# Optimization experiments

Measured on AMD Instinct MI355X. Metric: run time of the kernel, lower is better.

## Reference

```python
import jax, jax.numpy as jnp
import numpy as np


def setup_inputs() -> dict:
    key = jax.random.key(0)
    k1, k2 = jax.random.split(key)
    flow = jax.random.normal(k1, (4, 2, 256, 256), dtype=jnp.float32)   # [B,2,H,W] per-pixel flow over dt
    spike = jax.random.uniform(k2, (4, 64, 256, 256), dtype=jnp.float32)  # [B,C,H,W] spike voxel grid
    return {"flow": flow, "spike": spike}


def _splat(vals, xn, yn, H, W):
    """Forward bilinear splat of vals [H,W] to continuous coords (xn,yn) [H,W]."""
    x0 = jnp.floor(xn)
    y0 = jnp.floor(yn)
    wx = xn - x0  # fractional weights (differentiable w.r.t. flow)
    wy = yn - y0
    x0i = x0.astype(jnp.int32)
    y0i = y0.astype(jnp.int32)
    out = jnp.zeros(H * W, dtype=vals.dtype)
    corners = (
        (0, 0, (1.0 - wx) * (1.0 - wy)),
        (1, 0, wx * (1.0 - wy)),
        (0, 1, (1.0 - wx) * wy),
        (1, 1, wx * wy),
    )
    for dx, dy, w in corners:
        xi = x0i + dx
        yi = y0i + dy
        valid = (xi >= 0) & (xi < W) & (yi >= 0) & (yi < H)
        idx = jnp.clip(yi, 0, H - 1) * W + jnp.clip(xi, 0, W - 1)
        out = out.at[idx.ravel()].add(jnp.where(valid, w * vals, 0.0).ravel())
    return out.reshape(H, W)


def spike_warp_mid(spike, flow, dt):
    """Warp each time bin c by flow * (c - mid)/dt toward the middle timestamp (bilinear splat)."""
    B, C, H, W = spike.shape
    mid = (C - 1) / 2.0
    yy, xx = jnp.meshgrid(jnp.arange(H, dtype=spike.dtype),
                          jnp.arange(W, dtype=spike.dtype), indexing='ij')
    s = (jnp.arange(C, dtype=spike.dtype) - mid) / jnp.asarray(dt, spike.dtype)  # [C]
    u = flow[:, 0][:, None]  # [B,1,H,W]
    v = flow[:, 1][:, None]
    xn = xx + u * s[None, :, None, None]  # [B,C,H,W]
    yn = yy + v * s[None, :, None, None]
    splat_bc = jax.vmap(jax.vmap(lambda va, xa, ya: _splat(va, xa, ya, H, W)))
    return splat_bc(spike, xn, yn)  # [B,C,H,W]


def reference(flow, spike):
    B, C, H, W = spike.shape
    spike_warped = spike_warp_mid(spike, flow, dt=64)
    # Faithful to original: sum over BATCH dim inside per-batch loop (same each iter),
    # so loss = (B * -var) / B = -var(spike_image) with unbiased variance.
    spike_image = jnp.sum(spike_warped, axis=0)  # [C,H,W]
    loss = -jnp.var(spike_image - jnp.mean(spike_image), ddof=1)
    return loss
```

## Files before the change

### kernel.cpp

```cpp
#include <hip/hip_runtime.h>

typedef float f2 __attribute__((ext_vector_type(2)));
typedef float f4v __attribute__((ext_vector_type(4)));

constexpr int B = 4, C = 64, H = 256, W = 256;
constexpr int HW = H * W;
constexpr long long N_TOT = (long long)C * HW;

constexpr int TW = 16, TH = 8;
constexpr int SWX = 24, SWY = 16;
constexpr int SA = SWX * SWY;
constexpr int INW = 18, INH = 10;
constexpr int INA = INW * INH;
constexpr int OVW = 17, OVH = 9;
constexpr int OVA = OVW * OVH;
constexpr int NTIL = 512;
constexpr int NBLK = NTIL * 8;

__global__ __launch_bounds__(128) void fused_kernel(
    const float* __restrict__ flow,
    const float* __restrict__ spike,
    double* __restrict__ partials) {
  __shared__ __align__(16) f4v pl01[INA];
  __shared__ __align__(16) f4v pl23[INA];
  __shared__ f2 uvp[INA];
  __shared__ __align__(16) float ovf[8 * OVA];
  __shared__ double red[4];

  const int bid = blockIdx.x;
  const int tile = bid >> 3;
  const int m = bid & 7;
  const int tx0 = (tile & 15) * TW;
  const int ty0 = (tile >> 4) * TH;
  const int tid = threadIdx.x;
  const int qx = tid & 15, qy = tid >> 4;
  const int wave = tid >> 6;

  {
    f4v z = {0.f, 0.f, 0.f, 0.f};
    f4v* ov4 = (f4v*)ovf;
    for (int i = tid; i < (8 * OVA) / 4; i += 128) ov4[i] = z;
  }

  f2 smv[4];
#pragma unroll
  for (int t = 0; t < 4; ++t) {
    float s = ((float)(m + 8 * t) + 0.5f) * (1.0f / 64.0f);
    smv[t] = f2{-s, s};
  }
  const int cno[4] = {31 - m, 23 - m, 15 - m, 7 - m};
  const int cpo[4] = {32 + m, 40 + m, 48 + m, 56 + m};

  const int sbg = (ty0 - 4) * W + (tx0 - 4);

  int c_rc[3], c_meta[3];
#pragma unroll
  for (int k = 0; k < 3; ++k) {
    int pos = tid + 128 * k;
    int row = pos / SWX;
    int col = pos - row * SWX;
    int relx = col - 4, rely = row - 4;
    int gy = ty0 + rely, gx = tx0 + relx;
    bool val = ((unsigned)gy < 256u) & ((unsigned)gx < 256u);
    bool i0 = ((unsigned)(relx + 1) < 18u) & ((unsigned)(rely + 1) < 10u);
    bool i1 = ((unsigned)(relx + 2) < 20u) & ((unsigned)(rely + 2) < 12u);
    bool i2 = ((unsigned)(relx + 3) < 22u) & ((unsigned)(rely + 3) < 14u);
    c_rc[k] = (row << 8) | col;
    c_meta[k] = (int)val | ((int)i1 << 1) | ((int)i2 << 2) | ((int)i0 << 3);
  }

  float p_u[3], p_v[3];
  float4 p_a[3], p_b[3];

  auto prefetch = [&](int bb) {
    const float* fu = flow + (size_t)bb * 2 * HW;
    const float* fv = fu + HW;
    const float* spb = spike + (size_t)bb * C * HW;
#pragma unroll
    for (int k = 0; k < 3; ++k) {
      const int meta = c_meta[k];
      float u = 0.f, v = 0.f;
      float4 a = {0.f, 0.f, 0.f, 0.f};
      float4 d = {0.f, 0.f, 0.f, 0.f};
      if (meta & 1) {
        const int gp = sbg + c_rc[k];
        u = fu[gp];
        v = fv[gp];
        d.z = spb[(size_t)cno[3] * HW + gp];
        d.w = spb[(size_t)cpo[3] * HW + gp];
        if (meta & 8) { a.x = spb[(size_t)cno[0] * HW + gp];
                        a.y = spb[(size_t)cpo[0] * HW + gp]; }
        if (meta & 2) { a.z = spb[(size_t)cno[1] * HW + gp];
                        a.w = spb[(size_t)cpo[1] * HW + gp]; }
        if (meta & 4) { d.x = spb[(size_t)cno[2] * HW + gp];
                        d.y = spb[(size_t)cpo[2] * HW + gp]; }
      }
      p_u[k] = u; p_v[k] = v; p_a[k] = a; p_b[k] = d;
    }
  };

  prefetch(0);
  __syncthreads();

  const int qb = (qy + 1) * INW + (qx + 1);
  f2 acc2[4];
#pragma unroll
  for (int t = 0; t < 4; ++t) acc2[t] = f2{0.f, 0.f};

  for (int bb = 0; bb < B; ++bb) {
#pragma unroll
    for (int k = 0; k < 3; ++k) {
      const int meta = c_meta[k];
      const float u = p_u[k], v = p_v[k];
      const float4 a = p_a[k], d = p_b[k];
      const float es = fmaxf(fabsf(u), fabsf(v));
      const bool ev0 = es * smv[0].y >= 1.0f;
      const bool ev1 = es * smv[1].y >= 1.0f;
      const bool ev2 = es * smv[2].y >= 1.0f;
      const bool ev3 = es * smv[3].y >= 1.0f;
      const int row = c_rc[k] >> 8, col = c_rc[k] & 255;
      if (meta & 8) {
        const int ips = (row - 3) * INW + (col - 3);
        uvp[ips] = f2{u, v};
        pl01[ips] = f4v{ev0 ? 0.f : a.x, ev0 ? 0.f : a.y,
                        ev1 ? 0.f : a.z, ev1 ? 0.f : a.w};
        pl23[ips] = f4v{ev2 ? 0.f : d.x, ev2 ? 0.f : d.y,
                        ev3 ? 0.f : d.z, ev3 ? 0.f : d.w};
      }
      if (__any(ev3)) {
        const float px = (float)(col - 4), py = (float)(row - 4);
        const f2 u2 = f2{u, u}, v2 = f2{v, v};
        const f2 px2 = f2{px, px}, py2 = f2{py, py};
        const float nv[4] = {a.x, a.z, d.x, d.z};
        const float pv[4] = {a.y, a.w, d.y, d.w};
#pragma unroll
        for (int tt = 0; tt < 4; ++tt) {
          if (es * smv[tt].y >= 1.0f) {
            f2 xn = __builtin_elementwise_fma(u2, smv[tt], px2);
            f2 yn = __builtin_elementwise_fma(v2, smv[tt], py2);
#pragma unroll
            for (int h = 0; h < 2; ++h) {
              float x = xn[h], y = yn[h];
              float val = h ? pv[tt] : nv[tt];
              float fx = floorf(x), fy = floorf(y);
              float f = x - fx, g = y - fy;
              int X0 = (int)fx, Y0 = (int)fy;
              int ix0 = ((unsigned)X0 < 16u) ? X0 : 16;
              int ix1 = ((unsigned)(X0 + 1) < 16u) ? X0 + 1 : 16;
              int iy0 = ((unsigned)Y0 < 8u) ? Y0 : 8;
              int iy1 = ((unsigned)(Y0 + 1) < 8u) ? Y0 + 1 : 8;
              float* pl = &ovf[(2 * tt + h) * OVA];
              float w1 = f * val, w0 = val - w1;
              float g1 = g, g0 = 1.0f - g;
              atomicAdd(pl + iy0 * OVW + ix0, w0 * g0);
              atomicAdd(pl + iy0 * OVW + ix1, w1 * g0);
              atomicAdd(pl + iy1 * OVW + ix0, w0 * g1);
              atomicAdd(pl + iy1 * OVW + ix1, w1 * g1);
            }
          }
        }
      }
    }
    __syncthreads();
    if (bb + 1 < B) prefetch(bb + 1);

#pragma unroll
    for (int dy = -1; dy <= 1; ++dy) {
#pragma unroll
      for (int dx = -1; dx <= 1; ++dx) {
        const int ip = qb + dy * INW + dx;
        const f2 uvv = uvp[ip];
        const f4v A = pl01[ip];
        const f4v Bv = pl23[ip];
        const f2 u2 = f2{uvv.x, uvv.x};
        const f2 v2 = f2{uvv.y, uvv.y};
        const f2 vals[4] = {f2{A[0], A[1]}, f2{A[2], A[3]},
                            f2{Bv[0], Bv[1]}, f2{Bv[2], Bv[3]}};
#pragma unroll
        for (int tt = 0; tt < 4; ++tt) {
          const f2 dxv = u2 * smv[tt];
          const f2 dyv = v2 * smv[tt];
          f2 wx, wy;
          if (dx < 0)      wx = __builtin_elementwise_max(dxv, f2{0.f, 0.f});
          else if (dx > 0) wx = __builtin_elementwise_max(f2{0.f, 0.f} - dxv, f2{0.f, 0.f});
          else { wx.x = 1.0f - fabsf(dxv.x); wx.y = 1.0f - fabsf(dxv.y); }
          if (dy < 0)      wy = __builtin_elementwise_max(dyv, f2{0.f, 0.f});
          else if (dy > 0) wy = __builtin_elementwise_max(f2{0.f, 0.f} - dyv, f2{0.f, 0.f});
          else { wy.x = 1.0f - fabsf(dyv.x); wy.y = 1.0f - fabsf(dyv.y); }
          acc2[tt] = __builtin_elementwise_fma(wx * wy, vals[tt], acc2[tt]);
        }
      }
    }
    if (bb + 1 < B) __syncthreads();
  }

  const int oip = qy * OVW + qx;
#pragma unroll
  for (int tt = 0; tt < 4; ++tt) {
    acc2[tt] += f2{ovf[(2 * tt) * OVA + oip], ovf[(2 * tt + 1) * OVA + oip]};
  }

  double ls = 0.0, lq = 0.0;
#pragma unroll
  for (int tt = 0; tt < 4; ++tt) {
    double a = (double)acc2[tt].x, b2 = (double)acc2[tt].y;
    ls += a + b2;
    lq += a * a + b2 * b2;
  }
  for (int off = 32; off > 0; off >>= 1) {
    ls += __shfl_down(ls, off, 64);
    lq += __shfl_down(lq, off, 64);
  }
  if ((tid & 63) == 0) { red[wave * 2] = ls; red[wave * 2 + 1] = lq; }
  __syncthreads();
  if (tid == 0) {
    partials[2 * bid] = red[0] + red[2];
    partials[2 * bid + 1] = red[1] + red[3];
  }
}

__global__ __launch_bounds__(256) void finalize_kernel(
    const double* __restrict__ partials, float* __restrict__ out) {
  double s = 0.0, q = 0.0;
  for (int i = threadIdx.x; i < NBLK; i += 256) {
    s += partials[2 * i];
    q += partials[2 * i + 1];
  }
  for (int off = 32; off > 0; off >>= 1) {
    s += __shfl_down(s, off, 64);
    q += __shfl_down(q, off, 64);
  }
  __shared__ double ss[4], qq[4];
  int lane = threadIdx.x & 63;
  int wave = threadIdx.x >> 6;
  if (lane == 0) { ss[wave] = s; qq[wave] = q; }
  __syncthreads();
  if (threadIdx.x == 0) {
    double sum = ss[0] + ss[1] + ss[2] + ss[3];
    double sq = qq[0] + qq[1] + qq[2] + qq[3];
    double n = (double)N_TOT;
    double var = (sq - sum * sum / n) / (n - 1.0);
    out[0] = (float)(-var);
  }
}

extern "C" void kernel_launch(void* const* d_in, const int* in_sizes, int n_in,
                              void* d_out, int out_size, void* d_ws, size_t ws_size,
                              hipStream_t stream) {
  const float* flow = (const float*)d_in[0];
  const float* spike = (const float*)d_in[1];
  float* out = (float*)d_out;
  double* partials = (double*)d_ws;

  fused_kernel<<<dim3(NBLK), dim3(128), 0, stream>>>(flow, spike, partials);
  finalize_kernel<<<1, dim3(256), 0, stream>>>(partials, out);
}
```

Before: 154.9 us.

## Use single-wave 8x8 tiles to drop block barriers and load overflow spikes lazily

Shrinks each block from a 16x8 tile with two waves to an 8x8 tile handled by one 64-lane wave. All __syncthreads are replaced by explicit LDS waitcnts. The gather halo shrinks to a 10x10 ring. The scatter path for large displacements now loads spike values only for lanes that need them, instead of prefetching them for the whole 24x16 window. The cost is more blocks and a larger halo-to-tile ratio, and it relies on wave-synchronous LDS ordering being correct.

Measured after the change: 170.1 us. 9.8% more time.

```diff
diff --git a/kernel.cpp b/kernel.cpp
--- a/kernel.cpp
+++ b/kernel.cpp
@@ -7,169 +7,192 @@
 constexpr int HW = H * W;
 constexpr long long N_TOT = (long long)C * HW;
 
-constexpr int TW = 16, TH = 8;
-constexpr int SWX = 24, SWY = 16;
-constexpr int SA = SWX * SWY;
-constexpr int INW = 18, INH = 10;
-constexpr int INA = INW * INH;
-constexpr int OVW = 17, OVH = 9;
-constexpr int OVA = OVW * OVH;
-constexpr int NTIL = 512;
-constexpr int NBLK = NTIL * 8;
-
-__global__ __launch_bounds__(128) void fused_kernel(
+constexpr int QS = 8;
+constexpr int RNG = 10;
+constexpr int RNA = RNG * RNG;
+constexpr int OVP = 81;
+constexpr int NQ = 1024;
+constexpr int NBLK = NQ * 8;
+
+__global__ __launch_bounds__(64) void fused_kernel(
     const float* __restrict__ flow,
     const float* __restrict__ spike,
     double* __restrict__ partials) {
-  __shared__ __align__(16) f4v pl01[INA];
-  __shared__ __align__(16) f4v pl23[INA];
-  __shared__ f2 uvp[INA];
-  __shared__ __align__(16) float ovf[8 * OVA];
-  __shared__ double red[4];
+  __shared__ f2 uvr[RNA];
+  __shared__ __align__(16) f4v pl01[RNA];
+  __shared__ __align__(16) f4v pl23[RNA];
+  __shared__ float ovf[8 * OVP];
 
   const int bid = blockIdx.x;
-  const int tile = bid >> 3;
+  const int quad = bid >> 3;
   const int m = bid & 7;
-  const int tx0 = (tile & 15) * TW;
-  const int ty0 = (tile >> 4) * TH;
-  const int tid = threadIdx.x;
-  const int qx = tid & 15, qy = tid >> 4;
-  const int wave = tid >> 6;
+  const int qx0 = (quad & 31) * QS;
+  const int qy0 = (quad >> 5) * QS;
+  const int lane = threadIdx.x;
+  const int px = lane & 7, py = lane >> 3;
 
   {
     f4v z = {0.f, 0.f, 0.f, 0.f};
     f4v* ov4 = (f4v*)ovf;
-    for (int i = tid; i < (8 * OVA) / 4; i += 128) ov4[i] = z;
+#pragma unroll
+    for (int k = 0; k < 3; ++k) {
+      int i = lane + 64 * k;
+      if (i < (8 * OVP) / 4) ov4[i] = z;
+    }
   }
 
   f2 smv[4];
+  int cno[4], cpo[4];
 #pragma unroll
   for (int t = 0; t < 4; ++t) {
     float s = ((float)(m + 8 * t) + 0.5f) * (1.0f / 64.0f);
     smv[t] = f2{-s, s};
-  }
-  const int cno[4] = {31 - m, 23 - m, 15 - m, 7 - m};
-  const int cpo[4] = {32 + m, 40 + m, 48 + m, 56 + m};
-
-  const int sbg = (ty0 - 4) * W + (tx0 - 4);
-
-  int c_rc[3], c_meta[3];
-#pragma unroll
-  for (int k = 0; k < 3; ++k) {
-    int pos = tid + 128 * k;
-    int row = pos / SWX;
-    int col = pos - row * SWX;
-    int relx = col - 4, rely = row - 4;
-    int gy = ty0 + rely, gx = tx0 + relx;
-    bool val = ((unsigned)gy < 256u) & ((unsigned)gx < 256u);
-    bool i0 = ((unsigned)(relx + 1) < 18u) & ((unsigned)(rely + 1) < 10u);
-    bool i1 = ((unsigned)(relx + 2) < 20u) & ((unsigned)(rely + 2) < 12u);
-    bool i2 = ((unsigned)(relx + 3) < 22u) & ((unsigned)(rely + 3) < 14u);
-    c_rc[k] = (row << 8) | col;
-    c_meta[k] = (int)val | ((int)i1 << 1) | ((int)i2 << 2) | ((int)i0 << 3);
-  }
-
-  float p_u[3], p_v[3];
-  float4 p_a[3], p_b[3];
+    cno[t] = 31 - m - 8 * t;
+    cpo[t] = 32 + m + 8 * t;
+  }
+
+  int c_rgp[2];  bool c_rok[2];
+#pragma unroll
+  for (int k = 0; k < 2; ++k) {
+    int r = lane + 64 * k;
+    int rr = (r < RNA) ? r : 0;
+    int rely = rr / RNG - 1, relx = rr % RNG - 1;
+    int gy = qy0 + rely, gx = qx0 + relx;
+    bool ok = (r < RNA) & ((unsigned)gy < 256u) & ((unsigned)gx < 256u);
+    c_rgp[k] = (gy << 8) + gx;
+    c_rok[k] = ok;
+  }
+  int c_bgp[4];  bool c_bok[4];
+#pragma unroll
+  for (int k = 0; k < 4; ++k) {
+    int b = lane + 64 * k;
+    int rely = (b >> 4) - 4, relx = (b & 15) - 4;
+    int gy = qy0 + rely, gx = qx0 + relx;
+    bool ok = ((unsigned)gy < 256u) & ((unsigned)gx < 256u);
+    c_bgp[k] = (gy << 8) + gx;
+    c_bok[k] = ok;
+  }
+
+  float p_ru[2], p_rv[2];
+  float4 p_ra[2], p_rb[2];
+  float p_bu[4], p_bv[4];
 
   auto prefetch = [&](int bb) {
     const float* fu = flow + (size_t)bb * 2 * HW;
     const float* fv = fu + HW;
     const float* spb = spike + (size_t)bb * C * HW;
 #pragma unroll
-    for (int k = 0; k < 3; ++k) {
-      const int meta = c_meta[k];
+    for (int k = 0; k < 2; ++k) {
       float u = 0.f, v = 0.f;
       float4 a = {0.f, 0.f, 0.f, 0.f};
       float4 d = {0.f, 0.f, 0.f, 0.f};
-      if (meta & 1) {
-        const int gp = sbg + c_rc[k];
-        u = fu[gp];
-        v = fv[gp];
+      if (c_rok[k]) {
+        const int gp = c_rgp[k];
+        u = fu[gp]; v = fv[gp];
+        a.x = spb[(size_t)cno[0] * HW + gp];
+        a.y = spb[(size_t)cpo[0] * HW + gp];
+        a.z = spb[(size_t)cno[1] * HW + gp];
+        a.w = spb[(size_t)cpo[1] * HW + gp];
+        d.x = spb[(size_t)cno[2] * HW + gp];
+        d.y = spb[(size_t)cpo[2] * HW + gp];
         d.z = spb[(size_t)cno[3] * HW + gp];
         d.w = spb[(size_t)cpo[3] * HW + gp];
-        if (meta & 8) { a.x = spb[(size_t)cno[0] * HW + gp];
-                        a.y = spb[(size_t)cpo[0] * HW + gp]; }
-        if (meta & 2) { a.z = spb[(size_t)cno[1] * HW + gp];
-                        a.w = spb[(size_t)cpo[1] * HW + gp]; }
-        if (meta & 4) { d.x = spb[(size_t)cno[2] * HW + gp];
-                        d.y = spb[(size_t)cpo[2] * HW + gp]; }
-      }
-      p_u[k] = u; p_v[k] = v; p_a[k] = a; p_b[k] = d;
+      }
+      p_ru[k] = u; p_rv[k] = v; p_ra[k] = a; p_rb[k] = d;
+    }
+#pragma unroll
+    for (int k = 0; k < 4; ++k) {
+      float u = 0.f, v = 0.f;
+      if (c_bok[k]) {
+        const int gp = c_bgp[k];
+        u = fu[gp]; v = fv[gp];
+      }
+      p_bu[k] = u; p_bv[k] = v;
     }
   };
 
   prefetch(0);
-  __syncthreads();
-
-  const int qb = (qy + 1) * INW + (qx + 1);
+
   f2 acc2[4];
 #pragma unroll
   for (int t = 0; t < 4; ++t) acc2[t] = f2{0.f, 0.f};
 
   for (int bb = 0; bb < B; ++bb) {
 #pragma unroll
-    for (int k = 0; k < 3; ++k) {
-      const int meta = c_meta[k];
-      const float u = p_u[k], v = p_v[k];
-      const float4 a = p_a[k], d = p_b[k];
-      const float es = fmaxf(fabsf(u), fabsf(v));
-      const bool ev0 = es * smv[0].y >= 1.0f;
-      const bool ev1 = es * smv[1].y >= 1.0f;
-      const bool ev2 = es * smv[2].y >= 1.0f;
-      const bool ev3 = es * smv[3].y >= 1.0f;
-      const int row = c_rc[k] >> 8, col = c_rc[k] & 255;
-      if (meta & 8) {
-        const int ips = (row - 3) * INW + (col - 3);
-        uvp[ips] = f2{u, v};
-        pl01[ips] = f4v{ev0 ? 0.f : a.x, ev0 ? 0.f : a.y,
-                        ev1 ? 0.f : a.z, ev1 ? 0.f : a.w};
-        pl23[ips] = f4v{ev2 ? 0.f : d.x, ev2 ? 0.f : d.y,
-                        ev3 ? 0.f : d.z, ev3 ? 0.f : d.w};
-      }
-      if (__any(ev3)) {
-        const float px = (float)(col - 4), py = (float)(row - 4);
-        const f2 u2 = f2{u, u}, v2 = f2{v, v};
-        const f2 px2 = f2{px, px}, py2 = f2{py, py};
-        const float nv[4] = {a.x, a.z, d.x, d.z};
-        const float pv[4] = {a.y, a.w, d.y, d.w};
-#pragma unroll
-        for (int tt = 0; tt < 4; ++tt) {
-          if (es * smv[tt].y >= 1.0f) {
-            f2 xn = __builtin_elementwise_fma(u2, smv[tt], px2);
-            f2 yn = __builtin_elementwise_fma(v2, smv[tt], py2);
-#pragma unroll
-            for (int h = 0; h < 2; ++h) {
-              float x = xn[h], y = yn[h];
-              float val = h ? pv[tt] : nv[tt];
-              float fx = floorf(x), fy = floorf(y);
-              float f = x - fx, g = y - fy;
-              int X0 = (int)fx, Y0 = (int)fy;
-              int ix0 = ((unsigned)X0 < 16u) ? X0 : 16;
-              int ix1 = ((unsigned)(X0 + 1) < 16u) ? X0 + 1 : 16;
-              int iy0 = ((unsigned)Y0 < 8u) ? Y0 : 8;
-              int iy1 = ((unsigned)(Y0 + 1) < 8u) ? Y0 + 1 : 8;
-              float* pl = &ovf[(2 * tt + h) * OVA];
-              float w1 = f * val, w0 = val - w1;
-              float g1 = g, g0 = 1.0f - g;
-              atomicAdd(pl + iy0 * OVW + ix0, w0 * g0);
-              atomicAdd(pl + iy0 * OVW + ix1, w1 * g0);
-              atomicAdd(pl + iy1 * OVW + ix0, w0 * g1);
-              atomicAdd(pl + iy1 * OVW + ix1, w1 * g1);
+    for (int k = 0; k < 2; ++k) {
+      const int r = lane + 64 * k;
+      if (r < RNA) {
+        const float u = p_ru[k], v = p_rv[k];
+        const float4 a = p_ra[k], d = p_rb[k];
+        const float es = fmaxf(fabsf(u), fabsf(v));
+        const bool ev0 = es * smv[0].y >= 1.0f;
+        const bool ev1 = es * smv[1].y >= 1.0f;
+        const bool ev2 = es * smv[2].y >= 1.0f;
+        const bool ev3 = es * smv[3].y >= 1.0f;
+        uvr[r] = f2{u, v};
+        pl01[r] = f4v{ev0 ? 0.f : a.x, ev0 ? 0.f : a.y,
+                      ev1 ? 0.f : a.z, ev1 ? 0.f : a.w};
+        pl23[r] = f4v{ev2 ? 0.f : d.x, ev2 ? 0.f : d.y,
+                      ev3 ? 0.f : d.z, ev3 ? 0.f : d.w};
+      }
+    }
+
+    {
+      const float* spb = spike + (size_t)bb * C * HW;
+#pragma unroll
+      for (int k = 0; k < 4; ++k) {
+        const float u = p_bu[k], vv = p_bv[k];
+        const float es = fmaxf(fabsf(u), fabsf(vv));
+        const bool okl = c_bok[k];
+        if (__any(okl && (es * smv[3].y >= 1.0f))) {
+          const int b = lane + 64 * k;
+          const float pxc = (float)((b & 15) - 4);
+          const float pyc = (float)((b >> 4) - 4);
+          const f2 u2 = f2{u, u}, v2 = f2{vv, vv};
+          const f2 px2 = f2{pxc, pxc}, py2 = f2{pyc, pyc};
+          const int gp = c_bgp[k];
+#pragma unroll
+          for (int tt = 0; tt < 4; ++tt) {
+            if (okl && es * smv[tt].y >= 1.0f) {
+              const float vn = spb[(size_t)cno[tt] * HW + gp];
+              const float vp = spb[(size_t)cpo[tt] * HW + gp];
+              f2 xn = __builtin_elementwise_fma(u2, smv[tt], px2);
+              f2 yn = __builtin_elementwise_fma(v2, smv[tt], py2);
+#pragma unroll
+              for (int h = 0; h < 2; ++h) {
+                float x = xn[h], y = yn[h];
+                float val = h ? vp : vn;
+                float fx = floorf(x), fy = floorf(y);
+                float f = x - fx, g = y - fy;
+                int X0 = (int)fx, Y0 = (int)fy;
+                int ix0 = ((unsigned)X0 < 8u) ? X0 : 8;
+                int ix1 = ((unsigned)(X0 + 1) < 8u) ? X0 + 1 : 8;
+                int iy0 = ((unsigned)Y0 < 8u) ? Y0 : 8;
+                int iy1 = ((unsigned)(Y0 + 1) < 8u) ? Y0 + 1 : 8;
+                float* pl = &ovf[(2 * tt + h) * OVP];
+                float w1 = f * val, w0 = val - w1;
+                float g1 = g, g0 = 1.0f - g;
+                atomicAdd(pl + iy0 * 9 + ix0, w0 * g0);
+                atomicAdd(pl + iy0 * 9 + ix1, w1 * g0);
+                atomicAdd(pl + iy1 * 9 + ix0, w0 * g1);
+                atomicAdd(pl + iy1 * 9 + ix1, w1 * g1);
+              }
             }
           }
         }
       }
     }
-    __syncthreads();
+
     if (bb + 1 < B) prefetch(bb + 1);
 
+    asm volatile("s_waitcnt lgkmcnt(0)" ::: "memory");
+
 #pragma unroll
     for (int dy = -1; dy <= 1; ++dy) {
 #pragma unroll
       for (int dx = -1; dx <= 1; ++dx) {
-        const int ip = qb + dy * INW + dx;
-        const f2 uvv = uvp[ip];
+        const int ip = (py + 1 + dy) * RNG + (px + 1 + dx);
+        const f2 uvv = uvr[ip];
         const f4v A = pl01[ip];
         const f4v Bv = pl23[ip];
         const f2 u2 = f2{uvv.x, uvv.x};
@@ -191,13 +214,13 @@
         }
       }
     }
-    if (bb + 1 < B) __syncthreads();
-  }
-
-  const int oip = qy * OVW + qx;
+  }
+
+  asm volatile("s_waitcnt lgkmcnt(0)" ::: "memory");
+  const int oip = py * 9 + px;
 #pragma unroll
   for (int tt = 0; tt < 4; ++tt) {
-    acc2[tt] += f2{ovf[(2 * tt) * OVA + oip], ovf[(2 * tt + 1) * OVA + oip]};
+    acc2[tt] += f2{ovf[(2 * tt) * OVP + oip], ovf[(2 * tt + 1) * OVP + oip]};
   }
 
   double ls = 0.0, lq = 0.0;
@@ -211,11 +234,9 @@
     ls += __shfl_down(ls, off, 64);
     lq += __shfl_down(lq, off, 64);
   }
-  if ((tid & 63) == 0) { red[wave * 2] = ls; red[wave * 2 + 1] = lq; }
-  __syncthreads();
-  if (tid == 0) {
-    partials[2 * bid] = red[0] + red[2];
-    partials[2 * bid + 1] = red[1] + red[3];
+  if (lane == 0) {
+    partials[2 * bid] = ls;
+    partials[2 * bid + 1] = lq;
   }
 }
 
@@ -252,6 +273,6 @@
   float* out = (float*)d_out;
   double* partials = (double*)d_ws;
 
-  fused_kernel<<<dim3(NBLK), dim3(128), 0, stream>>>(flow, spike, partials);
+  fused_kernel<<<dim3(NBLK), dim3(64), 0, stream>>>(flow, spike, partials);
   finalize_kernel<<<1, dim3(256), 0, stream>>>(partials, out);
 }
```
